# Kernel optimization log

Measured on AMD Instinct MI355X. Metric: run time of the kernel, lower is better.

Reference implementation:

```python
import jax, jax.numpy as jnp
import numpy as np

K = 256
Q = 64
T = 500001  # length of return series r


def setup_inputs() -> dict:
    key = jax.random.key(0)
    k_r, k_b, k_w0, k_w = jax.random.split(key, 4)
    r = 0.01 * jax.random.normal(k_r, (T,), dtype=jnp.float32)
    a0 = jnp.float32(0.0)
    a1 = jnp.float32(0.0)
    raw_beta0 = jnp.float32(-4.0)
    raw_beta = (-4.0 + 0.1 * jax.random.normal(k_b, (K,))).astype(jnp.float32)
    raw_w0 = (-8.0 + 0.1 * jax.random.normal(k_w0, (K,))).astype(jnp.float32)
    raw_w = (-4.0 + 0.1 * jax.random.normal(k_w, (K, Q))).astype(jnp.float32)
    return {"r": r, "a0": a0, "a1": a1, "raw_beta0": raw_beta0,
            "raw_beta": raw_beta, "raw_w0": raw_w0, "raw_w": raw_w}


def reference(r, a0, a1, raw_beta0, raw_beta, raw_w0, raw_w):
    # AR(1) residuals
    u = r[1:] - a0 - a1 * r[:-1]          # [T-1]
    u2 = u * u                            # [T-1]
    n = u.shape[0]
    # init_u2 = unbiased variance of u2, repeated q times (torch.var default ddof=1)
    init_u2 = jnp.full((Q,), jnp.var(u2, ddof=1), dtype=u2.dtype)
    u2_full = jnp.concatenate([init_u2, u2])  # [q + T-1]
    # vectorized windowing: row t holds u2_full[t+q-1], ..., u2_full[t] (flipped window)
    t_idx = jnp.arange(n)[:, None]        # [n,1]
    lag_idx = jnp.arange(Q)[None, :]      # [1,q]
    idx = (Q + t_idx) - 1 - lag_idx       # [n,q]
    u2_lags = u2_full[idx]                # [n,q]
    # softplus-MLP volatility
    w0 = jax.nn.softplus(raw_w0)          # [k]
    w = jax.nn.softplus(raw_w)            # [k,q]
    h = jax.nn.relu(w0[None, :] + u2_lags @ w.T)  # [n,k]
    beta0 = jax.nn.softplus(raw_beta0)
    beta = jax.nn.softplus(raw_beta)      # [k]
    sigma2 = beta0 + h @ beta + 1e-8      # [n]
    # Gaussian negative log-likelihood
    nll = (0.5 * n * jnp.log(jnp.float32(2.0 * np.pi))
           + 0.5 * jnp.sum(jnp.log(sigma2))
           + 0.5 * jnp.sum(u2 / sigma2))
    return nll
```

## Files before the change

### kernel.cpp

```cpp
#include <hip/hip_runtime.h>
#include <math.h>

#define K_ 256
#define Q_ 64
#define NT 500000
#define NTILES (NT / 16)
#define TT_ 16
#define NBLK ((NT + 255) / 256)
#define GRID_MAIN ((NTILES + TT_ - 1) / TT_)

#define WS_BETA0  2
#define WS_U2     4
#define WS_U2B0   (WS_U2 + Q_ + NT)
#define WS_U2B1   (WS_U2B0 + (Q_ + NT + 1) / 2)
#define WS_BPACK  (WS_U2B1 + (Q_ + NT + 1) / 2)
#define WS_W0     (WS_BPACK + 8192)
#define WS_BETA   (WS_W0 + K_)
#define WS_PART   (WS_BETA + K_)
#define WS_PART2  (WS_PART + 2048)
#define WS_OUT    (WS_PART2 + 2048)

typedef __attribute__((ext_vector_type(8))) __bf16 bf16x8;
typedef __attribute__((ext_vector_type(4))) float  f32x4;

__device__ __forceinline__ float softplusf(float x) {
    return (x > 20.f) ? x : log1pf(__expf(x));
}

__device__ __forceinline__ unsigned short f2bf(float f) {
    unsigned int u = __float_as_uint(f);
    u = u + 0x7FFFu + ((u >> 16) & 1u);
    return (unsigned short)(u >> 16);
}

__global__ void k_u2(const float* __restrict__ r,
                     const float* __restrict__ a0p,
                     const float* __restrict__ a1p,
                     float* __restrict__ ws) {
    __shared__ float red[8];
    int i = blockIdx.x * blockDim.x + threadIdx.x;
    float a0 = a0p[0], a1 = a1p[0];
    float v = 0.f, v2 = 0.f;
    if (i < NT) {
        float u  = r[i + 1] - a0 - a1 * r[i];
        float u2 = u * u;
        ws[WS_U2 + Q_ + i] = u2;
        unsigned short b = f2bf(u2);
        ((unsigned short*)(ws + WS_U2B0))[Q_ + i]     = b;
        ((unsigned short*)(ws + WS_U2B1))[Q_ + i - 1] = b;
        v = u2; v2 = u2 * u2;
    }
    #pragma unroll
    for (int off = 32; off > 0; off >>= 1) {
        v  += __shfl_down(v,  off, 64);
        v2 += __shfl_down(v2, off, 64);
    }
    int wv = threadIdx.x >> 6;
    if ((threadIdx.x & 63) == 0) { red[wv * 2] = v; red[wv * 2 + 1] = v2; }
    __syncthreads();
    if (threadIdx.x == 0) {
        ws[WS_PART  + blockIdx.x] = red[0] + red[2] + red[4] + red[6];
        ws[WS_PART2 + blockIdx.x] = red[1] + red[3] + red[5] + red[7];
    }
}

__global__ void k_prep(const float* __restrict__ raw_beta0,
                       const float* __restrict__ raw_beta,
                       const float* __restrict__ raw_w0,
                       const float* __restrict__ raw_w,
                       float* __restrict__ ws) {
    int idx = blockIdx.x * blockDim.x + threadIdx.x;
    if (idx < 16384) {
        int jj = idx & 7, l = (idx >> 3) & 63, s = (idx >> 9) & 1, kc = idx >> 10;
        int j    = 32 * s + 8 * (l >> 4) + jj;
        int kout = kc * 16 + (l & 15);
        ((unsigned short*)(ws + WS_BPACK))[idx] =
            f2bf(softplusf(raw_w[kout * Q_ + (Q_ - 1 - j)]));
    } else if (idx < 16384 + K_) {
        int k = idx - 16384;
        ws[WS_W0 + k] = softplusf(raw_w0[k]);
    } else if (idx < 16384 + 2 * K_) {
        int k = idx - (16384 + K_);
        ws[WS_BETA + k] = softplusf(raw_beta[k]);
    } else if (idx < 16384 + 2 * K_ + Q_) {
        int j = idx - (16384 + 2 * K_);
        float s1 = 0.f, s2 = 0.f;
        for (int p = j; p < NBLK; p += 64) {
            s1 += ws[WS_PART  + p];
            s2 += ws[WS_PART2 + p];
        }
        #pragma unroll
        for (int mask = 1; mask < 64; mask <<= 1) {
            s1 += __shfl_xor(s1, mask, 64);
            s2 += __shfl_xor(s2, mask, 64);
        }
        float n  = (float)NT;
        float var = (s2 - s1 * s1 / n) / (n - 1.f);
        unsigned short b = f2bf(var);
        ((unsigned short*)(ws + WS_U2B0))[j] = b;
        if (j < Q_ - 1) ((unsigned short*)(ws + WS_U2B1))[j] = b;
        if (j == 0) ws[WS_BETA0] = softplusf(raw_beta0[0]);
    }
}

__launch_bounds__(256, 4)
__global__ void k_main(float* __restrict__ ws) {
    __shared__ __align__(16) float sig[TT_ * 256];
    __shared__ float red[4];

    int tid = threadIdx.x;
    int l = tid & 63, w = tid >> 6;
    int m = l & 15, q = l >> 4;

    const unsigned short* bp = (const unsigned short*)(ws + WS_BPACK);
    const float* u2f = ws + WS_U2;
    float beta0v = ws[WS_BETA0];

    bf16x8 Wf[4][2];
    f32x4 w0c[4], betc[4];
    #pragma unroll
    for (int i = 0; i < 4; ++i) {
        int kc = w * 4 + i;
        #pragma unroll
        for (int s = 0; s < 2; ++s)
            __builtin_memcpy(&Wf[i][s], bp + ((kc * 2 + s) * 64 + l) * 8, 16);
        w0c[i] = *(const f32x4*)(ws + WS_W0   + kc * 16 + q * 4);
        betc[i] = *(const f32x4*)(ws + WS_BETA + kc * 16 + q * 4);
    }

    int par = m & 1;
    const char* abase = (const char*)(ws + (par ? WS_U2B1 : WS_U2B0));
    int tile0 = blockIdx.x * TT_;
    int aoff = (tile0 * 16 + m + 8 * q - par) * 2;

    bf16x8 U0, U1, U0n, U1n;
    __builtin_memcpy(&U0, abase + aoff, 16);
    __builtin_memcpy(&U1, abase + aoff + 64, 16);

    #pragma unroll 2
    for (int it = 0; it < TT_; ++it) {
        int anext = aoff + 32;
        __builtin_memcpy(&U0n, abase + anext, 16);
        __builtin_memcpy(&U1n, abase + anext + 64, 16);

        float p[4];
        #pragma unroll
        for (int i = 0; i < 4; ++i) {
            f32x4 acc = __builtin_amdgcn_mfma_f32_16x16x32_bf16(Wf[i][0], U0, w0c[i], 0, 0, 0);
            acc = __builtin_amdgcn_mfma_f32_16x16x32_bf16(Wf[i][1], U1, acc, 0, 0, 0);
            float pi;
            pi = betc[i][0] * fmaxf(acc[0], 0.f);
            pi = fmaf(betc[i][1], fmaxf(acc[1], 0.f), pi);
            pi = fmaf(betc[i][2], fmaxf(acc[2], 0.f), pi);
            pi = fmaf(betc[i][3], fmaxf(acc[3], 0.f), pi);
            p[i] = pi;
        }
        sig[it * 256 + tid] = (p[0] + p[1]) + (p[2] + p[3]);

        aoff = anext; U0 = U0n; U1 = U1n;
    }

    __syncthreads();

    int tile = tid >> 4, tt = tid & 15;
    const float* sp = &sig[tile * 256 + tt];
    float s = 0.f;
    #pragma unroll
    for (int wq = 0; wq < 16; ++wq) s += sp[wq * 16];
    float sg = beta0v + s + 1e-8f;
    int t = tile0 * 16 + tid;
    float val = (t < NT) ? (__logf(sg) + u2f[Q_ + t] / sg) : 0.f;

    #pragma unroll
    for (int mask = 1; mask < 64; mask <<= 1)
        val += __shfl_xor(val, mask, 64);
    if (l == 0) red[w] = val;
    __syncthreads();
    if (tid == 0)
        ws[WS_OUT + blockIdx.x] = red[0] + red[1] + red[2] + red[3];
}

__global__ void k_final(const float* __restrict__ ws, float* __restrict__ out) {
    __shared__ float red[4];
    int tid = threadIdx.x;
    float s = 0.f;
    for (int p = tid; p < GRID_MAIN; p += 256) s += ws[WS_OUT + p];
    #pragma unroll
    for (int mask = 1; mask < 64; mask <<= 1)
        s += __shfl_xor(s, mask, 64);
    if ((tid & 63) == 0) red[tid >> 6] = s;
    __syncthreads();
    if (tid == 0)
        out[0] = 0.5f * (float)NT * 1.8378770664093453f
               + 0.5f * (red[0] + red[1] + red[2] + red[3]);
}

extern "C" void kernel_launch(void* const* d_in, const int* in_sizes, int n_in,
                              void* d_out, int out_size, void* d_ws, size_t ws_size,
                              hipStream_t stream) {
    const float* r        = (const float*)d_in[0];
    const float* a0       = (const float*)d_in[1];
    const float* a1       = (const float*)d_in[2];
    const float* raw_b0   = (const float*)d_in[3];
    const float* raw_beta = (const float*)d_in[4];
    const float* raw_w0   = (const float*)d_in[5];
    const float* raw_w    = (const float*)d_in[6];
    float* out = (float*)d_out;
    float* ws  = (float*)d_ws;

    k_u2<<<NBLK, 256, 0, stream>>>(r, a0, a1, ws);

    int prep_threads = 16384 + 2 * K_ + Q_;
    k_prep<<<(prep_threads + 255) / 256, 256, 0, stream>>>(
        raw_b0, raw_beta, raw_w0, raw_w, ws);

    k_main<<<GRID_MAIN, 256, 0, stream>>>(ws);

    k_final<<<1, 256, 0, stream>>>(ws, out);
}
```

Before: 103.6 us.

## Fuse final reduction into main kernel, drop fp32 u2 buffer, vectorize u2 pass

The residual pass now handles 8 elements per thread with vector loads and writes only the two bf16 shifted copies, no longer storing an fp32 u2 array. The main kernel recomputes u from r in its epilogue, processes 32 tiles per block, and uses an atomic counter so the last block does the final reduction, removing the k_final launch. This cuts memory traffic and one kernel launch. In exchange it adds a memset, a threadfence/atomic sequence, and larger per-block shared memory, which may lower occupancy.

```diff
diff --git a/kernel.cpp b/kernel.cpp
--- a/kernel.cpp
+++ b/kernel.cpp
@@ -5,20 +5,22 @@
 #define Q_ 64
 #define NT 500000
 #define NTILES (NT / 16)
-#define TT_ 16
-#define NBLK ((NT + 255) / 256)
+#define TT_ 32
 #define GRID_MAIN ((NTILES + TT_ - 1) / TT_)
+#define NSUM 245
 
 #define WS_BETA0  2
-#define WS_U2     4
-#define WS_U2B0   (WS_U2 + Q_ + NT)
-#define WS_U2B1   (WS_U2B0 + (Q_ + NT + 1) / 2)
-#define WS_BPACK  (WS_U2B1 + (Q_ + NT + 1) / 2)
+#define WS_U2B0   4
+#define U2ELEMS   (Q_ + NT + 16)
+#define U2F       ((U2ELEMS + 1) / 2)
+#define WS_U2B1   (WS_U2B0 + U2F)
+#define WS_BPACK  (WS_U2B1 + U2F)
 #define WS_W0     (WS_BPACK + 8192)
 #define WS_BETA   (WS_W0 + K_)
 #define WS_PART   (WS_BETA + K_)
-#define WS_PART2  (WS_PART + 2048)
-#define WS_OUT    (WS_PART2 + 2048)
+#define WS_PART2  (WS_PART + 512)
+#define WS_OUT    (WS_PART2 + 512)
+#define WS_CNT    (WS_OUT + 1024)
 
 typedef __attribute__((ext_vector_type(8))) __bf16 bf16x8;
 typedef __attribute__((ext_vector_type(4))) float  f32x4;
@@ -33,22 +35,34 @@
     return (unsigned short)(u >> 16);
 }
 
-__global__ void k_u2(const float* __restrict__ r,
-                     const float* __restrict__ a0p,
-                     const float* __restrict__ a1p,
-                     float* __restrict__ ws) {
+__global__ void k_sum(const float* __restrict__ r,
+                      const float* __restrict__ a0p,
+                      const float* __restrict__ a1p,
+                      float* __restrict__ ws) {
     __shared__ float red[8];
-    int i = blockIdx.x * blockDim.x + threadIdx.x;
+    int i0 = (blockIdx.x * 256 + threadIdx.x) * 8;
     float a0 = a0p[0], a1 = a1p[0];
     float v = 0.f, v2 = 0.f;
-    if (i < NT) {
-        float u  = r[i + 1] - a0 - a1 * r[i];
-        float u2 = u * u;
-        ws[WS_U2 + Q_ + i] = u2;
-        unsigned short b = f2bf(u2);
-        ((unsigned short*)(ws + WS_U2B0))[Q_ + i]     = b;
-        ((unsigned short*)(ws + WS_U2B1))[Q_ + i - 1] = b;
-        v = u2; v2 = u2 * u2;
+    if (i0 < NT) {
+        float rr[9];
+        *(float4*)&rr[0] = *(const float4*)(r + i0);
+        *(float4*)&rr[4] = *(const float4*)(r + i0 + 4);
+        rr[8] = r[i0 + 8];
+        unsigned short bs[8];
+        #pragma unroll
+        for (int j = 0; j < 8; ++j) {
+            float u  = rr[j + 1] - a0 - a1 * rr[j];
+            float u2 = u * u;
+            bs[j] = f2bf(u2);
+            v += u2;
+            v2 = fmaf(u2, u2, v2);
+        }
+        unsigned short* b0 = (unsigned short*)(ws + WS_U2B0);
+        unsigned short* b1 = (unsigned short*)(ws + WS_U2B1);
+        __builtin_memcpy(b0 + Q_ + i0, bs, 16);
+        b1[Q_ - 1 + i0] = bs[0];
+        __builtin_memcpy(b1 + Q_ + i0, bs + 1, 12);
+        b1[Q_ + i0 + 6] = bs[7];
     }
     #pragma unroll
     for (int off = 32; off > 0; off >>= 1) {
@@ -85,7 +99,8 @@
     } else if (idx < 16384 + 2 * K_ + Q_) {
         int j = idx - (16384 + 2 * K_);
         float s1 = 0.f, s2 = 0.f;
-        for (int p = j; p < NBLK; p += 64) {
+        #pragma unroll
+        for (int p = j; p < NSUM; p += 64) {
             s1 += ws[WS_PART  + p];
             s2 += ws[WS_PART2 + p];
         }
@@ -104,17 +119,21 @@
 }
 
 __launch_bounds__(256, 4)
-__global__ void k_main(float* __restrict__ ws) {
+__global__ void k_main(const float* __restrict__ r,
+                       const float* __restrict__ a0p,
+                       const float* __restrict__ a1p,
+                       float* __restrict__ ws, float* __restrict__ out) {
     __shared__ __align__(16) float sig[TT_ * 256];
     __shared__ float red[4];
+    __shared__ int lastflag;
 
     int tid = threadIdx.x;
     int l = tid & 63, w = tid >> 6;
     int m = l & 15, q = l >> 4;
 
     const unsigned short* bp = (const unsigned short*)(ws + WS_BPACK);
-    const float* u2f = ws + WS_U2;
     float beta0v = ws[WS_BETA0];
+    float a0 = a0p[0], a1 = a1p[0];
 
     bf16x8 Wf[4][2];
     f32x4 w0c[4], betc[4];
@@ -124,14 +143,13 @@
         #pragma unroll
         for (int s = 0; s < 2; ++s)
             __builtin_memcpy(&Wf[i][s], bp + ((kc * 2 + s) * 64 + l) * 8, 16);
-        w0c[i] = *(const f32x4*)(ws + WS_W0   + kc * 16 + q * 4);
+        w0c[i]  = *(const f32x4*)(ws + WS_W0   + kc * 16 + q * 4);
         betc[i] = *(const f32x4*)(ws + WS_BETA + kc * 16 + q * 4);
     }
 
     int par = m & 1;
     const char* abase = (const char*)(ws + (par ? WS_U2B1 : WS_U2B0));
-    int tile0 = blockIdx.x * TT_;
-    int aoff = (tile0 * 16 + m + 8 * q - par) * 2;
+    int aoff = (blockIdx.x * 512 + m + 8 * q - par) * 2;
 
     bf16x8 U0, U1, U0n, U1n;
     __builtin_memcpy(&U0, abase + aoff, 16);
@@ -162,37 +180,48 @@
 
     __syncthreads();
 
-    int tile = tid >> 4, tt = tid & 15;
-    const float* sp = &sig[tile * 256 + tt];
-    float s = 0.f;
-    #pragma unroll
-    for (int wq = 0; wq < 16; ++wq) s += sp[wq * 16];
-    float sg = beta0v + s + 1e-8f;
-    int t = tile0 * 16 + tid;
-    float val = (t < NT) ? (__logf(sg) + u2f[Q_ + t] / sg) : 0.f;
-
+    float val = 0.f;
+    #pragma unroll
+    for (int rep = 0; rep < 2; ++rep) {
+        int lt = tid + rep * 256;
+        int tile = lt >> 4, tt = lt & 15;
+        const float* sp = &sig[tile * 256 + tt];
+        float s = 0.f;
+        #pragma unroll
+        for (int wq = 0; wq < 16; ++wq) s += sp[wq * 16];
+        float sg = beta0v + s + 1e-8f;
+        int t = blockIdx.x * 512 + lt;
+        if (t < NT) {
+            float u  = r[t + 1] - a0 - a1 * r[t];
+            val += __logf(sg) + (u * u) / sg;
+        }
+    }
     #pragma unroll
     for (int mask = 1; mask < 64; mask <<= 1)
         val += __shfl_xor(val, mask, 64);
     if (l == 0) red[w] = val;
     __syncthreads();
-    if (tid == 0)
+
+    if (tid == 0) {
         ws[WS_OUT + blockIdx.x] = red[0] + red[1] + red[2] + red[3];
-}
-
-__global__ void k_final(const float* __restrict__ ws, float* __restrict__ out) {
-    __shared__ float red[4];
-    int tid = threadIdx.x;
-    float s = 0.f;
-    for (int p = tid; p < GRID_MAIN; p += 256) s += ws[WS_OUT + p];
-    #pragma unroll
-    for (int mask = 1; mask < 64; mask <<= 1)
-        s += __shfl_xor(s, mask, 64);
-    if ((tid & 63) == 0) red[tid >> 6] = s;
-    __syncthreads();
-    if (tid == 0)
-        out[0] = 0.5f * (float)NT * 1.8378770664093453f
-               + 0.5f * (red[0] + red[1] + red[2] + red[3]);
+        __threadfence();
+        unsigned old = atomicAdd((unsigned*)(ws + WS_CNT), 1u);
+        lastflag = (old == GRID_MAIN - 1);
+    }
+    __syncthreads();
+    if (lastflag) {
+        __threadfence();
+        float s = 0.f;
+        for (int p = tid; p < GRID_MAIN; p += 256) s += ws[WS_OUT + p];
+        #pragma unroll
+        for (int mask = 1; mask < 64; mask <<= 1)
+            s += __shfl_xor(s, mask, 64);
+        if (l == 0) red[w] = s;
+        __syncthreads();
+        if (tid == 0)
+            out[0] = 0.5f * (float)NT * 1.8378770664093453f
+                   + 0.5f * (red[0] + red[1] + red[2] + red[3]);
+    }
 }
 
 extern "C" void kernel_launch(void* const* d_in, const int* in_sizes, int n_in,
@@ -208,13 +237,13 @@
     float* out = (float*)d_out;
     float* ws  = (float*)d_ws;
 
-    k_u2<<<NBLK, 256, 0, stream>>>(r, a0, a1, ws);
+    hipMemsetAsync(ws + WS_CNT, 0, 4, stream);
+
+    k_sum<<<NSUM, 256, 0, stream>>>(r, a0, a1, ws);
 
     int prep_threads = 16384 + 2 * K_ + Q_;
     k_prep<<<(prep_threads + 255) / 256, 256, 0, stream>>>(
         raw_b0, raw_beta, raw_w0, raw_w, ws);
 
-    k_main<<<GRID_MAIN, 256, 0, stream>>>(ws);
-
-    k_final<<<1, 256, 0, stream>>>(ws, out);
-}
+    k_main<<<GRID_MAIN, 256, 0, stream>>>(r, a0, a1, ws, out);
+}
```

Measured after the change: 107.3 us. 1.04x slower.
